# Kernel tuning notes

Measured on AMD Instinct MI355X. Metric: run time of the kernel, lower is better.

The kernel has to match this reference:

```python
import jax, jax.numpy as jnp
import numpy as np

D_MODEL = 1024
N_HEADS = 16
D_FF = 4096
N_EXPERTS = 8
B, S = 4, 1024
HEAD_DIM = D_MODEL // N_HEADS

# H4 simple roots (normalized), fixed buffer
_PHI = (1.0 + np.sqrt(5.0)) / 2.0
_R = np.array([[1, -1, 0, 0], [0, 1, -1, 0], [0, 0, 1, 0], [-0.5, 0.5, 0.5, _PHI / 2]], dtype=np.float32)
_R = _R / np.linalg.norm(_R, axis=1, keepdims=True)
ROOTS = jnp.asarray(_R)  # (4, 4)

# chamber -> (expert1, expert2) lookup, fixed buffer
_P = []
for i in range(16):
    e1 = i % N_EXPERTS
    e2 = (i // 2 + 1) % N_EXPERTS
    if e1 == e2:
        e2 = (e2 + 1) % N_EXPERTS
    _P.append([e1, e2])
CHAMBER_TO_EXPERTS = jnp.asarray(np.array(_P, dtype=np.int32))  # (16, 2)


def layer_norm(x, g, b, eps=1e-5):
    mu = jnp.mean(x, axis=-1, keepdims=True)
    var = jnp.mean(jnp.square(x - mu), axis=-1, keepdims=True)
    return (x - mu) / jnp.sqrt(var + eps) * g + b


def ternary_linear(x, w):
    # ternary quantization with STE; forward uses quantized weights
    alpha = jnp.mean(jnp.abs(w))
    w_tern = jnp.sign(w) * (jnp.abs(w) > 0.5 * alpha).astype(w.dtype)
    w_q = w + jax.lax.stop_gradient(w_tern - w)
    # per-token RMS normalization of the input
    rms = jnp.linalg.norm(x, axis=-1, keepdims=True) / np.sqrt(x.shape[-1])
    x_norm = x / (rms + 1e-8)
    return x_norm @ w_q.T


def setup_inputs() -> dict:
    key = jax.random.key(0)
    ks = jax.random.split(key, 8)
    init = lambda k, shape: jax.random.normal(k, shape, jnp.float32) * 0.02
    return {
        "x": jax.random.normal(ks[0], (B, S, D_MODEL), jnp.float32),
        "g1": jnp.ones((D_MODEL,), jnp.float32),
        "b1": jnp.zeros((D_MODEL,), jnp.float32),
        "g2": jnp.ones((D_MODEL,), jnp.float32),
        "b2": jnp.zeros((D_MODEL,), jnp.float32),
        "in_w": init(ks[1], (3 * D_MODEL, D_MODEL)),
        "in_b": jnp.zeros((3 * D_MODEL,), jnp.float32),
        "out_w": init(ks[2], (D_MODEL, D_MODEL)),
        "out_b": jnp.zeros((D_MODEL,), jnp.float32),
        "router_w": init(ks[3], (4, D_MODEL)),
        "up_w": init(ks[4], (N_EXPERTS, D_FF, D_MODEL)),
        "down_w": init(ks[5], (N_EXPERTS, D_MODEL, D_FF)),
    }


def reference(x, g1, b1, g2, b2, in_w, in_b, out_w, out_b, router_w, up_w, down_w):
    batch, seq, d = x.shape

    # ---- attention sublayer ----
    residual = x
    h = layer_norm(x, g1, b1)
    qkv = h @ in_w.T + in_b  # (B,S,3D)
    q, k, v = jnp.split(qkv, 3, axis=-1)
    def heads(t):
        return t.reshape(batch, seq, N_HEADS, HEAD_DIM).transpose(0, 2, 1, 3)
    q, k, v = heads(q), heads(k), heads(v)
    scores = jnp.einsum("bhqd,bhkd->bhqk", q, k) / np.sqrt(HEAD_DIM)
    attn = jax.nn.softmax(scores, axis=-1)
    o = jnp.einsum("bhqk,bhkd->bhqd", attn, v)
    o = o.transpose(0, 2, 1, 3).reshape(batch, seq, d)
    x = o @ out_w.T + out_b + residual

    # ---- MoE sublayer ----
    residual = x
    x_norm = layer_norm(x, g2, b2)

    # geometric router
    h4 = x_norm @ router_w.T  # (B,S,4)
    h4 = h4 / jnp.maximum(jnp.linalg.norm(h4, axis=-1, keepdims=True), 1e-12)
    dots = h4 @ ROOTS.T  # (B,S,4)
    bits = (dots >= 0).astype(jnp.int32)
    chamber = bits[..., 0] + 2 * bits[..., 1] + 4 * bits[..., 2] + 8 * bits[..., 3]
    expert_idx = CHAMBER_TO_EXPERTS[chamber]  # (B,S,2)
    confidence = jnp.min(jnp.abs(dots), axis=-1)
    w1 = 0.5 + 0.3 * jax.nn.sigmoid(confidence)
    w2 = 1.0 - w1

    # dense masked combine: per-token weight is 0 for non-routed experts,
    # so this computes the same math as the masked gather/scatter loop
    out = jnp.zeros_like(x_norm)
    for e in range(N_EXPERTS):
        w_e = w1 * (expert_idx[..., 0] == e) + w2 * (expert_idx[..., 1] == e)  # (B,S)
        h_e = ternary_linear(x_norm, up_w[e])
        h_e = jax.nn.gelu(h_e, approximate=False)
        y_e = ternary_linear(h_e, down_w[e])
        out = out + y_e * w_e[..., None]

    return out + residual
```

## Files before the change

### kernel.cpp

```cpp
#include <hip/hip_runtime.h>
#include <math.h>

#define TOK 4096
#define DM 1024
#define DFF 4096
#define MATSZ 4194304
#define PADROWS 9216
#define PADTILES 72

typedef unsigned short u16;
typedef unsigned int   u32;
typedef __attribute__((ext_vector_type(8))) __bf16 bf16x8;
typedef __attribute__((ext_vector_type(4))) float  f32x4;
typedef __attribute__((ext_vector_type(4))) int    i32x4;
typedef __attribute__((ext_vector_type(4))) float  f4v;

#define GLD16(gp, lp) __builtin_amdgcn_global_load_lds( \
    (const __attribute__((address_space(1))) void*)(gp), \
    (__attribute__((address_space(3))) void*)(lp), 16, 0, 0)

__device__ __forceinline__ float b2f(u16 u){ return __uint_as_float(((u32)u)<<16); }
__device__ __forceinline__ u16 f2b(float f){
  u32 i = __float_as_uint(f);
  u32 r = i + 0x7fffu + ((i>>16)&1u);
  return (u16)(r>>16);
}
__device__ __forceinline__ void unpack8(uint4 rw, float* dst){
  u32 u0=rw.x,u1=rw.y,u2=rw.z,u3=rw.w;
  dst[0]=__uint_as_float(u0<<16); dst[1]=__uint_as_float(u0&0xffff0000u);
  dst[2]=__uint_as_float(u1<<16); dst[3]=__uint_as_float(u1&0xffff0000u);
  dst[4]=__uint_as_float(u2<<16); dst[5]=__uint_as_float(u2&0xffff0000u);
  dst[6]=__uint_as_float(u3<<16); dst[7]=__uint_as_float(u3&0xffff0000u);
}
__device__ __forceinline__ float block_reduce_sum256(float v, float* red){
  #pragma unroll
  for (int off=32; off>0; off>>=1) v += __shfl_down(v, off);
  __syncthreads();
  if ((threadIdx.x & 63)==0) red[threadIdx.x>>6] = v;
  __syncthreads();
  return red[0]+red[1]+red[2]+red[3];
}
__device__ __forceinline__ float block_reduce_max256(float v, float* red){
  #pragma unroll
  for (int off=32; off>0; off>>=1) v = fmaxf(v, __shfl_down(v, off));
  __syncthreads();
  if ((threadIdx.x & 63)==0) red[threadIdx.x>>6] = v;
  __syncthreads();
  return fmaxf(fmaxf(red[0],red[1]), fmaxf(red[2],red[3]));
}

__global__ __launch_bounds__(256) void k_absum1(const float* __restrict__ up, const float* __restrict__ dn,
                                                float* __restrict__ partials){
  const int b = blockIdx.x;
  const size_t f4i = (size_t)b*2048;
  const f4v* s4 = (b < 4096) ? ((const f4v*)up + f4i) : ((const f4v*)dn + (f4i - 8388608));
  const int tid = threadIdx.x;
  float a0=0.f,a1=0.f,a2=0.f,a3=0.f;
  #pragma unroll
  for (int i=0;i<2;i++){
    f4v v0 = __builtin_nontemporal_load(s4 + i*1024 + tid);
    f4v v1 = __builtin_nontemporal_load(s4 + i*1024 + tid + 256);
    f4v v2 = __builtin_nontemporal_load(s4 + i*1024 + tid + 512);
    f4v v3 = __builtin_nontemporal_load(s4 + i*1024 + tid + 768);
    a0 += fabsf(v0[0])+fabsf(v0[1])+fabsf(v0[2])+fabsf(v0[3]);
    a1 += fabsf(v1[0])+fabsf(v1[1])+fabsf(v1[2])+fabsf(v1[3]);
    a2 += fabsf(v2[0])+fabsf(v2[1])+fabsf(v2[2])+fabsf(v2[3]);
    a3 += fabsf(v3[0])+fabsf(v3[1])+fabsf(v3[2])+fabsf(v3[3]);
  }
  __shared__ float red[4];
  float tot = block_reduce_sum256((a0+a1)+(a2+a3), red);
  if (tid==0) partials[b]=tot;
}
__global__ void k_absum2(const float* __restrict__ partials, float* __restrict__ thr,
                         int* __restrict__ counts, int* __restrict__ counts2){
  const int t=threadIdx.x;
  const int m=t>>4, k=t&15;
  float s=0.f;
  for (int i=0;i<32;i++) s += partials[m*512 + k + i*16];
  s += __shfl_xor(s,1); s += __shfl_xor(s,2); s += __shfl_xor(s,4); s += __shfl_xor(s,8);
  if (k==0) thr[m]=0.5f*s/4194304.0f;
  if (t>=224 && t<232) counts[t-224]=0;
  if (t>=232 && t<240) counts2[t-232]=0;
}
__global__ __launch_bounds__(256) void k_ternarize(const float* __restrict__ up, const float* __restrict__ dn,
                                                   const float* __restrict__ thr, signed char* __restrict__ tern){
  const int nvec = 16777216;
  for (int i0 = blockIdx.x*1024 + threadIdx.x; i0 < nvec; i0 += gridDim.x*1024){
    const int i1 = i0 + 256, i2 = i0 + 512, i3 = i0 + 768;
    f4v w0 = (i0 < 8388608) ? __builtin_nontemporal_load((const f4v*)up + i0) : __builtin_nontemporal_load((const f4v*)dn + (i0-8388608));
    f4v w1 = (i1 < 8388608) ? __builtin_nontemporal_load((const f4v*)up + i1) : __builtin_nontemporal_load((const f4v*)dn + (i1-8388608));
    f4v w2 = (i2 < 8388608) ? __builtin_nontemporal_load((const f4v*)up + i2) : __builtin_nontemporal_load((const f4v*)dn + (i2-8388608));
    f4v w3 = (i3 < 8388608) ? __builtin_nontemporal_load((const f4v*)up + i3) : __builtin_nontemporal_load((const f4v*)dn + (i3-8388608));
    float t0 = thr[(int)(((size_t)i0*4)>>22)];
    float t1 = thr[(int)(((size_t)i1*4)>>22)];
    float t2 = thr[(int)(((size_t)i2*4)>>22)];
    float t3 = thr[(int)(((size_t)i3*4)>>22)];
    char4 c0, c1, c2, c3;
    c0.x=(fabsf(w0[0])>t0)?(w0[0]>0.f?1:-1):0; c0.y=(fabsf(w0[1])>t0)?(w0[1]>0.f?1:-1):0;
    c0.z=(fabsf(w0[2])>t0)?(w0[2]>0.f?1:-1):0; c0.w=(fabsf(w0[3])>t0)?(w0[3]>0.f?1:-1):0;
    c1.x=(fabsf(w1[0])>t1)?(w1[0]>0.f?1:-1):0; c1.y=(fabsf(w1[1])>t1)?(w1[1]>0.f?1:-1):0;
    c1.z=(fabsf(w1[2])>t1)?(w1[2]>0.f?1:-1):0; c1.w=(fabsf(w1[3])>t1)?(w1[3]>0.f?1:-1):0;
    c2.x=(fabsf(w2[0])>t2)?(w2[0]>0.f?1:-1):0; c2.y=(fabsf(w2[1])>t2)?(w2[1]>0.f?1:-1):0;
    c2.z=(fabsf(w2[2])>t2)?(w2[2]>0.f?1:-1):0; c2.w=(fabsf(w2[3])>t2)?(w2[3]>0.f?1:-1):0;
    c3.x=(fabsf(w3[0])>t3)?(w3[0]>0.f?1:-1):0; c3.y=(fabsf(w3[1])>t3)?(w3[1]>0.f?1:-1):0;
    c3.z=(fabsf(w3[2])>t3)?(w3[2]>0.f?1:-1):0; c3.w=(fabsf(w3[3])>t3)?(w3[3]>0.f?1:-1):0;
    *(char4*)(tern+(size_t)i0*4) = c0;
    *(char4*)(tern+(size_t)i1*4) = c1;
    *(char4*)(tern+(size_t)i2*4) = c2;
    *(char4*)(tern+(size_t)i3*4) = c3;
  }
}
__global__ __launch_bounds__(256) void k_f2b(const float* __restrict__ s, u16* __restrict__ d, int n4){
  int i = blockIdx.x*256+threadIdx.x;
  if (i<n4){
    float4 v=((const float4*)s)[i];
    ushort4 o; o.x=f2b(v.x); o.y=f2b(v.y); o.z=f2b(v.z); o.w=f2b(v.w);
    ((ushort4*)d)[i]=o;
  }
}

__global__ __launch_bounds__(256) void k_ln1(const float* __restrict__ x, const float* __restrict__ g,
                                             const float* __restrict__ b, u16* __restrict__ h){
  __shared__ float red[4];
  const int t=blockIdx.x, tid=threadIdx.x;
  float4 xv = ((const float4*)(x + (size_t)t*DM))[tid];
  float s  = xv.x+xv.y+xv.z+xv.w;
  float sq = xv.x*xv.x+xv.y*xv.y+xv.z*xv.z+xv.w*xv.w;
  float sum  = block_reduce_sum256(s, red);
  float sums = block_reduce_sum256(sq, red);
  float mu = sum*(1.0f/DM);
  float var = sums*(1.0f/DM) - mu*mu;
  float rstd = rsqrtf(var+1e-5f);
  float4 gv = ((const float4*)g)[tid];
  float4 bv = ((const float4*)b)[tid];
  ushort4 pk;
  pk.x = f2b((xv.x-mu)*rstd*gv.x+bv.x);
  pk.y = f2b((xv.y-mu)*rstd*gv.y+bv.y);
  pk.z = f2b((xv.z-mu)*rstd*gv.z+bv.z);
  pk.w = f2b((xv.w-mu)*rstd*gv.w+bv.w);
  ((ushort4*)(h + (size_t)t*DM))[tid] = pk;
}

template<int MODE>
__global__ __launch_bounds__(256) void k_gemm(const u16* __restrict__ A, const u16* __restrict__ B,
                                              int K, int ldc, const float* __restrict__ bias,
                                              const float* __restrict__ resid, void* __restrict__ Cout,
                                              u16* __restrict__ vT){
  __shared__ u16 As[2][128*32];
  __shared__ u16 Bs[2][128*32];
  const int tid = threadIdx.x;
  const int w = tid>>6, lane = tid&63;
  const int m0 = blockIdx.y*128, n0 = blockIdx.x*128;

  const int sr = lane>>2, ss = lane&3;
  const int ra0 = w*32 + sr, ra1 = ra0 + 16;
  const int kb0 = (ss ^ ((ra0>>1)&3))<<3;
  const int kb1 = (ss ^ ((ra1>>1)&3))<<3;
  const u16* pa0 = A + (size_t)(m0+ra0)*K + kb0;
  const u16* pa1 = A + (size_t)(m0+ra1)*K + kb1;
  const u16* pb0 = B + (size_t)(n0+ra0)*K + kb0;
  const u16* pb1 = B + (size_t)(n0+ra1)*K + kb1;
  const int lo0 = (w*32)*32, lo1 = lo0 + 16*32;

  const int wm = w>>1, wn = w&1;
  const int lr = lane&15, sl = lane>>4;
  int offA[4], offB[4];
  #pragma unroll
  for (int m=0;m<4;m++){ int r = wm*64 + m*16 + lr; offA[m] = r*64 + ((sl ^ ((r>>1)&3))<<4); }
  #pragma unroll
  for (int n=0;n<4;n++){ int r = wn*64 + n*16 + lr; offB[n] = r*64 + ((sl ^ ((r>>1)&3))<<4); }

  f32x4 acc[4][4] = {};
  const int NT = K>>5;
  GLD16(pa0, &As[0][lo0]); GLD16(pa1, &As[0][lo1]);
  GLD16(pb0, &Bs[0][lo0]); GLD16(pb1, &Bs[0][lo1]);
  pa0+=32; pa1+=32; pb0+=32; pb1+=32;
  __syncthreads();

  for (int t=0;t<NT;t++){
    if (t+1<NT){
      const int nb=(t+1)&1;
      GLD16(pa0, &As[nb][lo0]); GLD16(pa1, &As[nb][lo1]);
      GLD16(pb0, &Bs[nb][lo0]); GLD16(pb1, &Bs[nb][lo1]);
      pa0+=32; pa1+=32; pb0+=32; pb1+=32;
    }
    const char* Ab = (const char*)As[t&1];
    const char* Bb = (const char*)Bs[t&1];
    bf16x8 af[4], bfv[4];
    #pragma unroll
    for (int m=0;m<4;m++) af[m] = *(const bf16x8*)(Ab + offA[m]);
    #pragma unroll
    for (int n=0;n<4;n++) bfv[n] = *(const bf16x8*)(Bb + offB[n]);
    #pragma unroll
    for (int m=0;m<4;m++)
      #pragma unroll
      for (int n=0;n<4;n++)
        acc[m][n] = __builtin_amdgcn_mfma_f32_16x16x32_bf16(af[m], bfv[n], acc[m][n], 0, 0, 0);
    __syncthreads();
  }

  const int rowg = lane>>4;
  #pragma unroll
  for (int m=0;m<4;m++){
    const int rbase = m0 + wm*64 + m*16 + rowg*4;
    #pragma unroll
    for (int n=0;n<4;n++){
      const int col = n0 + wn*64 + n*16 + lr;
      if (MODE==2){
        u16 pk4[4];
        #pragma unroll
        for (int j=0;j<4;j++){
          float v = acc[m][n][j] + bias[col];
          pk4[j] = f2b(v);
          ((u16*)Cout)[(size_t)(rbase+j)*ldc + col] = pk4[j];
        }
        if (col >= 2048){
          const int d = col-2048, hd = d>>6, dd = d&63;
          const int bb = rbase>>10, s = rbase&1023;
          uint2 pk; pk.x = (u32)pk4[0] | ((u32)pk4[1]<<16); pk.y = (u32)pk4[2] | ((u32)pk4[3]<<16);
          *(uint2*)(vT + (((size_t)((bb*16+hd)*64+dd))<<10) + s) = pk;
        }
      } else {
        #pragma unroll
        for (int j=0;j<4;j++){
          const size_t ci = (size_t)(rbase+j)*ldc + col;
          ((float*)Cout)[ci] = acc[m][n][j] + bias[col] + resid[ci];
        }
      }
    }
  }
}

template<bool GATHER>
__global__ __launch_bounds__(256) void k_gemm8(const signed char* __restrict__ A, const signed char* __restrict__ Ball,
                                               int K, int ldc,
                                               const int* __restrict__ tile2e, const int* __restrict__ rowmap,
                                               const float* __restrict__ rscale, u16* __restrict__ Cout){
  int e = tile2e[blockIdx.y];
  if (e < 0) return;
  const signed char* Bp = Ball + (size_t)e * MATSZ;
  __shared__ signed char As[2][128*64];
  __shared__ signed char Bs[2][128*64];
  const int tid = threadIdx.x;
  const int w = tid>>6, lane = tid&63;
  const int m0 = blockIdx.y*128, n0 = blockIdx.x*128;

  const int sr = lane>>2, ss = lane&3;
  const int ra0 = w*32 + sr, ra1 = ra0 + 16;
  const int kb0 = (ss ^ ((ra0>>1)&3))<<4;
  const int kb1 = (ss ^ ((ra1>>1)&3))<<4;
  const signed char *pa0, *pa1;
  if (GATHER){
    int t0 = rowmap[m0+ra0]; if (t0<0) t0 = 0;
    int t1 = rowmap[m0+ra1]; if (t1<0) t1 = 0;
    pa0 = A + (size_t)t0*K + kb0;
    pa1 = A + (size_t)t1*K + kb1;
  } else {
    pa0 = A + (size_t)(m0+ra0)*K + kb0;
    pa1 = A + (size_t)(m0+ra1)*K + kb1;
  }
  const signed char* pb0 = Bp + (size_t)(n0+ra0)*K + kb0;
  const signed char* pb1 = Bp + (size_t)(n0+ra1)*K + kb1;
  const int lo0 = (w*32)*64, lo1 = lo0 + 16*64;

  const int wm = w>>1, wn = w&1;
  const int lr = lane&15, sl = lane>>4;
  int offA[4], offB[4];
  #pragma unroll
  for (int m=0;m<4;m++){ int r = wm*64 + m*16 + lr; offA[m] = r*64 + ((sl ^ ((r>>1)&3))<<4); }
  #pragma unroll
  for (int n=0;n<4;n++){ int r = wn*64 + n*16 + lr; offB[n] = r*64 + ((sl ^ ((r>>1)&3))<<4); }

  i32x4 acc[4][4] = {};
  const int NT = K>>6;
  GLD16(pa0, &As[0][lo0]); GLD16(pa1, &As[0][lo1]);
  GLD16(pb0, &Bs[0][lo0]); GLD16(pb1, &Bs[0][lo1]);
  pa0+=64; pa1+=64; pb0+=64; pb1+=64;
  __syncthreads();

  for (int t=0;t<NT;t++){
    if (t+1<NT){
      const int nb=(t+1)&1;
      GLD16(pa0, &As[nb][lo0]); GLD16(pa1, &As[nb][lo1]);
      GLD16(pb0, &Bs[nb][lo0]); GLD16(pb1, &Bs[nb][lo1]);
      pa0+=64; pa1+=64; pb0+=64; pb1+=64;
    }
    const char* Ab = (const char*)As[t&1];
    const char* Bb = (const char*)Bs[t&1];
    i32x4 af[4], bfv[4];
    #pragma unroll
    for (int m=0;m<4;m++) af[m] = *(const i32x4*)(Ab + offA[m]);
    #pragma unroll
    for (int n=0;n<4;n++) bfv[n] = *(const i32x4*)(Bb + offB[n]);
    #pragma unroll
    for (int m=0;m<4;m++)
      #pragma unroll
      for (int n=0;n<4;n++)
        acc[m][n] = __builtin_amdgcn_mfma_i32_16x16x64_i8(af[m], bfv[n], acc[m][n], 0, 0, 0);
    __syncthreads();
  }

  const int rowg = lane>>4;
  #pragma unroll
  for (int m=0;m<4;m++){
    const int rbase = m0 + wm*64 + m*16 + rowg*4;
    #pragma unroll
    for (int n=0;n<4;n++){
      const int col = n0 + wn*64 + n*16 + lr;
      #pragma unroll
      for (int j=0;j<4;j++){
        float v = (float)acc[m][n][j] * rscale[rbase+j];
        Cout[(size_t)(rbase+j)*ldc + col] = f2b(v);
      }
    }
  }
}

__global__ __launch_bounds__(256) void k_attn_mfma(const u16* __restrict__ qkv, const u16* __restrict__ vT,
                                                   u16* __restrict__ ob){
  __shared__ u16 Ks[2][64*64];
  __shared__ u16 Vs[2][64*64];
  __shared__ u16 Pa[4*16*64];
  const int qt=blockIdx.x, hh=blockIdx.y, bb=blockIdx.z;
  const int tid=threadIdx.x, w=tid>>6, lane=tid&63;
  const int g=lane>>4, lr=lane&15;
  const int srow8=lane>>3, sslot=lane&7;
  const float RTHR = 11.5f;

  bf16x8 qa[2];
  {
    const u16* qp = qkv + ((size_t)(bb*1024 + qt*64 + w*16 + lr))*3072 + hh*64 + g*8;
    #pragma unroll
    for (int c=0;c<2;c++){
      uint4 raw = *(const uint4*)(qp + c*32);
      float tv[8]; unpack8(raw,tv);
      union { u16 s[8]; bf16x8 v; } qq;
      #pragma unroll
      for (int i=0;i<8;i++) qq.s[i] = f2b(tv[i]*0.18033688f);
      qa[c] = qq.v;
    }
  }

  float mrow[4], lrow[4];
  #pragma unroll
  for (int j=0;j<4;j++){ mrow[j]=-1e30f; lrow[j]=0.f; }
  f32x4 acc_o[4] = {};

  char* pbuf = (char*)Pa + (w<<11);

  const int row0 = w*16 + srow8, row1 = row0 + 8;
  const int fs0 = (sslot ^ (row0&7))<<3;
  const int fs1 = (sslot ^ (row1&7))<<3;
  const int ldso0 = (w*16)*64, ldso1 = (w*16+8)*64;

  {
    const u16* gk0 = qkv + ((size_t)(bb*1024 + row0))*3072 + 1024 + hh*64 + fs0;
    const u16* gk1 = qkv + ((size_t)(bb*1024 + row1))*3072 + 1024 + hh*64 + fs1;
    GLD16(gk0, &Ks[0][ldso0]); GLD16(gk1, &Ks[0][ldso1]);
    const u16* gv0 = vT + ((size_t)((bb*16+hh)*64 + row0))*1024 + fs0;
    const u16* gv1 = vT + ((size_t)((bb*16+hh)*64 + row1))*1024 + fs1;
    GLD16(gv0, &Vs[0][ldso0]); GLD16(gv1, &Vs[0][ldso1]);
  }
  __syncthreads();

  for (int kt=0; kt<16; ++kt){
    if (kt+1<16){
      const int nb=(kt+1)&1;
      const u16* gk0 = qkv + ((size_t)(bb*1024 + (kt+1)*64 + row0))*3072 + 1024 + hh*64 + fs0;
      const u16* gk1 = qkv + ((size_t)(bb*1024 + (kt+1)*64 + row1))*3072 + 1024 + hh*64 + fs1;
      GLD16(gk0, &Ks[nb][ldso0]); GLD16(gk1, &Ks[nb][ldso1]);
      const u16* gv0 = vT + ((size_t)((bb*16+hh)*64 + row0))*1024 + (kt+1)*64 + fs0;
      const u16* gv1 = vT + ((size_t)((bb*16+hh)*64 + row1))*1024 + (kt+1)*64 + fs1;
      GLD16(gv0, &Vs[nb][ldso0]); GLD16(gv1, &Vs[nb][ldso1]);
    }
    const char* Kb = (const char*)Ks[kt&1];
    const char* Vb = (const char*)Vs[kt&1];

    f32x4 sacc[4] = {};
    #pragma unroll
    for (int ct=0; ct<4; ct++){
      const int kv = ct*16 + lr;
      const char* krow = Kb + kv*128;
      bf16x8 kb0 = *(const bf16x8*)(krow + (((g  ) ^ (kv&7))<<4));
      bf16x8 kb1 = *(const bf16x8*)(krow + (((4+g) ^ (kv&7))<<4));
      sacc[ct] = __builtin_amdgcn_mfma_f32_16x16x32_bf16(qa[0], kb0, sacc[ct], 0,0,0);
      sacc[ct] = __builtin_amdgcn_mfma_f32_16x16x32_bf16(qa[1], kb1, sacc[ct], 0,0,0);
    }

    float vmx[4]; bool okl = true;
    #pragma unroll
    for (int j=0;j<4;j++){
      vmx[j] = fmaxf(fmaxf(sacc[0][j],sacc[1][j]), fmaxf(sacc[2][j],sacc[3][j]));
      okl = okl && (vmx[j]-mrow[j] <= RTHR);
    }
    float psum[4] = {0.f,0.f,0.f,0.f};
    if (__all((int)okl)){
      #pragma unroll
      for (int ct=0; ct<4; ct++){
        #pragma unroll
        for (int j=0;j<4;j++){
          float p = exp2f(sacc[ct][j]-mrow[j]);
          psum[j] += p;
          const int q = g*4+j, k = ct*16+lr;
          *(u16*)(pbuf + q*128 + (((k>>3) ^ (q&7))<<4) + ((k&7)<<1)) = f2b(p);
        }
      }
      #pragma unroll
      for (int j=0;j<4;j++){
        float s = psum[j];
        s += __shfl_xor(s,1); s += __shfl_xor(s,2); s += __shfl_xor(s,4); s += __shfl_xor(s,8);
        lrow[j] += s;
      }
    } else {
      float mnew[4], corr[4];
      #pragma unroll
      for (int j=0;j<4;j++){
        float v = vmx[j];
        v = fmaxf(v, __shfl_xor(v,1));
        v = fmaxf(v, __shfl_xor(v,2));
        v = fmaxf(v, __shfl_xor(v,4));
        v = fmaxf(v, __shfl_xor(v,8));
        mnew[j] = fmaxf(mrow[j], v);
        corr[j] = exp2f(mrow[j]-mnew[j]);
        mrow[j] = mnew[j];
      }
      #pragma unroll
      for (int ct=0; ct<4; ct++){
        #pragma unroll
        for (int j=0;j<4;j++){
          float p = exp2f(sacc[ct][j]-mrow[j]);
          psum[j] += p;
          const int q = g*4+j, k = ct*16+lr;
          *(u16*)(pbuf + q*128 + (((k>>3) ^ (q&7))<<4) + ((k&7)<<1)) = f2b(p);
        }
      }
      #pragma unroll
      for (int j=0;j<4;j++){
        float s = psum[j];
        s += __shfl_xor(s,1); s += __shfl_xor(s,2); s += __shfl_xor(s,4); s += __shfl_xor(s,8);
        lrow[j] = lrow[j]*corr[j] + s;
      }
      #pragma unroll
      for (int ctd=0; ctd<4; ctd++)
        #pragma unroll
        for (int j=0;j<4;j++) acc_o[ctd][j] *= corr[j];
    }

    #pragma unroll
    for (int c=0;c<2;c++){
      bf16x8 pa = *(const bf16x8*)(pbuf + lr*128 + (((c*4+g) ^ (lr&7))<<4));
      #pragma unroll
      for (int ctd=0; ctd<4; ctd++){
        const int d = ctd*16 + lr;
        bf16x8 vb = *(const bf16x8*)(Vb + d*128 + (((c*4+g) ^ (d&7))<<4));
        acc_o[ctd] = __builtin_amdgcn_mfma_f32_16x16x32_bf16(pa, vb, acc_o[ctd], 0,0,0);
      }
    }
    __syncthreads();
  }

  #pragma unroll
  for (int j=0;j<4;j++){
    const float inv = 1.0f/lrow[j];
    const int row = bb*1024 + qt*64 + w*16 + g*4 + j;
    u16* op = ob + (size_t)row*DM + hh*64 + lr;
    #pragma unroll
    for (int ctd=0; ctd<4; ctd++) op[ctd*16] = f2b(acc_o[ctd][j]*inv);
  }
}

__global__ __launch_bounds__(256) void k_ln2_router(const float* __restrict__ xa, const float* __restrict__ g,
                                                    const float* __restrict__ b, const float* __restrict__ rw,
                                                    signed char* __restrict__ xn8, int* __restrict__ eidx,
                                                    float* __restrict__ w1o, float* __restrict__ sbc){
  __shared__ float red[4];
  const int t=blockIdx.x, tid=threadIdx.x;
  float4 xv = ((const float4*)(xa + (size_t)t*DM))[tid];
  float s  = xv.x+xv.y+xv.z+xv.w;
  float sq = xv.x*xv.x+xv.y*xv.y+xv.z*xv.z+xv.w*xv.w;
  float sum  = block_reduce_sum256(s, red);
  float sums = block_reduce_sum256(sq, red);
  float mu = sum*(1.0f/DM);
  float var = sums*(1.0f/DM) - mu*mu;
  float rstd = rsqrtf(var+1e-5f);
  float4 gv = ((const float4*)g)[tid];
  float4 bv = ((const float4*)b)[tid];
  float y0=(xv.x-mu)*rstd*gv.x+bv.x;
  float y1=(xv.y-mu)*rstd*gv.y+bv.y;
  float y2=(xv.z-mu)*rstd*gv.z+bv.z;
  float y3=(xv.w-mu)*rstd*gv.w+bv.w;
  float4 r0=((const float4*)(rw+0*DM))[tid];
  float4 r1=((const float4*)(rw+1*DM))[tid];
  float4 r2=((const float4*)(rw+2*DM))[tid];
  float4 r3=((const float4*)(rw+3*DM))[tid];
  float nsq = y0*y0+y1*y1+y2*y2+y3*y3;
  float d0 = y0*r0.x+y1*r0.y+y2*r0.z+y3*r0.w;
  float d1 = y0*r1.x+y1*r1.y+y2*r1.z+y3*r1.w;
  float d2 = y0*r2.x+y1*r2.y+y2*r2.z+y3*r2.w;
  float d3 = y0*r3.x+y1*r3.y+y2*r3.z+y3*r3.w;
  float am = fmaxf(fmaxf(fabsf(y0),fabsf(y1)), fmaxf(fabsf(y2),fabsf(y3)));
  float AM = block_reduce_max256(am, red);
  float SQ = block_reduce_sum256(nsq, red);
  float D0 = block_reduce_sum256(d0, red);
  float D1 = block_reduce_sum256(d1, red);
  float D2 = block_reduce_sum256(d2, red);
  float D3 = block_reduce_sum256(d3, red);
  float qs = fmaxf(AM, 1e-12f) * (1.0f/127.0f);
  float inv = 1.0f/qs;
  char4 c;
  c.x = (signed char)__float2int_rn(y0*inv);
  c.y = (signed char)__float2int_rn(y1*inv);
  c.z = (signed char)__float2int_rn(y2*inv);
  c.w = (signed char)__float2int_rn(y3*inv);
  ((char4*)(xn8 + (size_t)t*DM))[tid] = c;
  if (tid==0){
    float n = fmaxf(sqrtf(D0*D0+D1*D1+D2*D2+D3*D3), 1e-12f);
    float h0=D0/n, h1=D1/n, h2=D2/n, h3=D3/n;
    float dot0 = 0.70710678f*(h0-h1);
    float dot1 = 0.70710678f*(h1-h2);
    float dot2 = h2;
    float dot3 = (-0.5f*h0+0.5f*h1+0.5f*h2+0.80901699f*h3)*0.8437966f;
    int ch = (int)(dot0>=0.f) + 2*(int)(dot1>=0.f) + 4*(int)(dot2>=0.f) + 8*(int)(dot3>=0.f);
    int e1 = ch & 7;
    int e2 = ((ch>>1)+1) & 7;
    if (e1==e2) e2=(e2+1)&7;
    float conf = fminf(fminf(fabsf(dot0),fabsf(dot1)), fminf(fabsf(dot2),fabsf(dot3)));
    eidx[2*t]=e1; eidx[2*t+1]=e2;
    w1o[t]=0.5f + 0.3f/(1.0f+__expf(-conf));
    sbc[t]= qs / (sqrtf(SQ*(1.0f/DM))+1e-8f);
  }
}

__global__ void k_count(const int* __restrict__ eidx, int* __restrict__ counts){
  int t = blockIdx.x*256+threadIdx.x;
  if (t<TOK){ atomicAdd(&counts[eidx[2*t]],1); atomicAdd(&counts[eidx[2*t+1]],1); }
}
__global__ void k_offsets(const int* __restrict__ counts, int* __restrict__ offs, int* __restrict__ tile2e,
                          int* __restrict__ rowmap, float* __restrict__ srow, int* __restrict__ ptot){
  const int tid=threadIdx.x;
  if (tid==0){
    int off=0;
    for (int e=0;e<8;e++){
      offs[e]=off;
      int pad = ((counts[e]+127)>>7)<<7;
      int t0=off>>7, t1=(off+pad)>>7;
      for (int tt=t0;tt<t1;tt++) tile2e[tt]=e;
      off+=pad;
    }
    offs[8]=off; *ptot=off;
    for (int tt=off>>7; tt<PADTILES; tt++) tile2e[tt]=-1;
  }
  for (int i=tid;i<PADROWS;i+=blockDim.x){ rowmap[i]=-1; srow[i]=0.f; }
}
__global__ void k_scatter(const int* __restrict__ eidx, const int* __restrict__ offs, int* __restrict__ counts2,
                          int* __restrict__ rowmap, int* __restrict__ tokrow,
                          const float* __restrict__ sbc, float* __restrict__ srow){
  int t = blockIdx.x*256+threadIdx.x;
  if (t<TOK){
    int e1=eidx[2*t], e2=eidx[2*t+1];
    float s = sbc[t];
    int p1 = atomicAdd(&counts2[e1],1);
    int r1 = offs[e1]+p1; rowmap[r1]=t; srow[r1]=s; tokrow[2*t]=r1;
    int p2 = atomicAdd(&counts2[e2],1);
    int r2 = offs[e2]+p2; rowmap[r2]=t; srow[r2]=s; tokrow[2*t+1]=r2;
  }
}

__global__ __launch_bounds__(256) void k_gelu_rms(const u16* __restrict__ he, signed char* __restrict__ he8,
                                                  float* __restrict__ qd, const int* __restrict__ ptot){
  const int row = blockIdx.x;
  if (row >= *ptot) return;
  const u16* p = he + (size_t)row*DFF;
  const int tid=threadIdx.x;
  uint4 rw0 = ((const uint4*)p)[2*tid];
  uint4 rw1 = ((const uint4*)p)[2*tid+1];
  float v[16];
  unpack8(rw0, v); unpack8(rw1, v+8);
  float sq=0.f;
  #pragma unroll
  for (int q=0;q<16;q++){
    float xg = v[q];
    float ge = 0.5f*xg*(1.0f+erff(xg*0.70710678f));
    v[q]=ge; sq += ge*ge;
  }
  __shared__ float red[4];
  float SQ = block_reduce_sum256(sq, red);
  float s = 1.0f/(sqrtf(SQ*(1.0f/DFF))+1e-8f);
  float am = 0.f;
  #pragma unroll
  for (int q=0;q<16;q++){ v[q]*=s; am = fmaxf(am, fabsf(v[q])); }
  float AM = block_reduce_max256(am, red);
  float q8 = fmaxf(AM, 1e-12f) * (1.0f/127.0f);
  float inv = 1.0f/q8;
  union { signed char c[16]; uint4 u; } pk;
  #pragma unroll
  for (int q=0;q<16;q++) pk.c[q] = (signed char)__float2int_rn(v[q]*inv);
  ((uint4*)(he8 + (size_t)row*DFF))[tid] = pk.u;
  if (tid==0) qd[row] = q8;
}

__global__ __launch_bounds__(256) void k_combine(const float* __restrict__ xa, const u16* __restrict__ y,
                                                 const int* __restrict__ tokrow, const float* __restrict__ w1,
                                                 float* __restrict__ out){
  const int t=blockIdx.x, tid=threadIdx.x;
  const int r1=tokrow[2*t], r2=tokrow[2*t+1];
  const float a = w1[t], bw = 1.0f-a;
  float4 xv = ((const float4*)(xa + (size_t)t*DM))[tid];
  ushort4 y1 = ((const ushort4*)(y + (size_t)r1*DM))[tid];
  ushort4 y2 = ((const ushort4*)(y + (size_t)r2*DM))[tid];
  float4 o;
  o.x = xv.x + a*b2f(y1.x) + bw*b2f(y2.x);
  o.y = xv.y + a*b2f(y1.y) + bw*b2f(y2.y);
  o.z = xv.z + a*b2f(y1.z) + bw*b2f(y2.z);
  o.w = xv.w + a*b2f(y1.w) + bw*b2f(y2.w);
  ((float4*)(out + (size_t)t*DM))[tid] = o;
}

extern "C" void kernel_launch(void* const* d_in, const int* in_sizes, int n_in,
                              void* d_out, int out_size, void* d_ws, size_t ws_size,
                              hipStream_t stream){
  (void)in_sizes; (void)n_in; (void)out_size; (void)ws_size;
  const float* x    = (const float*)d_in[0];
  const float* g1   = (const float*)d_in[1];
  const float* b1   = (const float*)d_in[2];
  const float* g2   = (const float*)d_in[3];
  const float* b2   = (const float*)d_in[4];
  const float* in_w = (const float*)d_in[5];
  const float* in_b = (const float*)d_in[6];
  const float* out_w= (const float*)d_in[7];
  const float* out_b= (const float*)d_in[8];
  const float* rw   = (const float*)d_in[9];
  const float* up_w = (const float*)d_in[10];
  const float* dn_w = (const float*)d_in[11];
  float* out = (float*)d_out;

  char* base = (char*)d_ws; size_t off=0;
  auto alloc = [&](size_t bytes)->char*{ char* p = base+off; off=(off+bytes+255)&~(size_t)255; return p; };
  u16* h      = (u16*)alloc((size_t)TOK*DM*2);
  u16* qkv    = (u16*)alloc((size_t)TOK*3072*2);
  u16* ob     = (u16*)alloc((size_t)TOK*DM*2);
  float* xattn= (float*)alloc((size_t)TOK*DM*4);
  signed char* xn8 = (signed char*)alloc((size_t)TOK*DM);
  signed char* tern8 = (signed char*)alloc((size_t)16*MATSZ);
  u16* wbf_in = (u16*)alloc((size_t)3145728*2);
  u16* wbf_out= (u16*)alloc((size_t)1048576*2);
  u16* vT     = (u16*)alloc((size_t)4*16*64*1024*2);
  u16* he     = (u16*)alloc((size_t)PADROWS*DFF*2);
  signed char* he8 = (signed char*)alloc((size_t)PADROWS*DFF);
  u16* y      = (u16*)alloc((size_t)PADROWS*DM*2);
  float* partials = (float*)alloc(8192*4);
  float* thr  = (float*)alloc(64);
  int* counts = (int*)alloc(32);
  int* counts2= (int*)alloc(32);
  int* offs   = (int*)alloc(64);
  int* ptot   = (int*)alloc(64);
  int* eidx   = (int*)alloc((size_t)TOK*2*4);
  float* w1b  = (float*)alloc((size_t)TOK*4);
  float* sbc  = (float*)alloc((size_t)TOK*4);
  float* srow = (float*)alloc((size_t)PADROWS*4);
  float* qd   = (float*)alloc((size_t)PADROWS*4);
  int* tokrow = (int*)alloc((size_t)TOK*2*4);
  int* rowmap = (int*)alloc((size_t)PADROWS*4);
  int* tile2e = (int*)alloc(PADTILES*4);

  k_absum1<<<8192,256,0,stream>>>(up_w, dn_w, partials);
  k_absum2<<<1,256,0,stream>>>(partials, thr, counts, counts2);
  k_ternarize<<<8192,256,0,stream>>>(up_w, dn_w, thr, tern8);
  k_f2b<<<3072,256,0,stream>>>(in_w, wbf_in, 786432);
  k_f2b<<<1024,256,0,stream>>>(out_w, wbf_out, 262144);
  k_ln1<<<TOK,256,0,stream>>>(x, g1, b1, h);
  k_gemm<2><<<dim3(24,32),256,0,stream>>>(h, wbf_in, 1024, 3072, in_b, nullptr, qkv, vT);
  k_attn_mfma<<<dim3(16,16,4),256,0,stream>>>(qkv, vT, ob);
  k_gemm<3><<<dim3(8,32),256,0,stream>>>(ob, wbf_out, 1024, 1024, out_b, x, xattn, nullptr);
  k_ln2_router<<<TOK,256,0,stream>>>(xattn, g2, b2, rw, xn8, eidx, w1b, sbc);
  k_count<<<16,256,0,stream>>>(eidx, counts);
  k_offsets<<<1,256,0,stream>>>(counts, offs, tile2e, rowmap, srow, ptot);
  k_scatter<<<16,256,0,stream>>>(eidx, offs, counts2, rowmap, tokrow, sbc, srow);
  k_gemm8<true><<<dim3(32,PADTILES),256,0,stream>>>(xn8, tern8, 1024, 4096,
      tile2e, rowmap, srow, he);
  k_gelu_rms<<<PADROWS,256,0,stream>>>(he, he8, qd, ptot);
  k_gemm8<false><<<dim3(8,PADTILES),256,0,stream>>>(he8, tern8 + (size_t)8*MATSZ, 4096, 1024,
      tile2e, nullptr, qd, y);
  k_combine<<<TOK,256,0,stream>>>(xattn, y, tokrow, w1b, out);
}
```

Baseline: 497.8 us.

## Triple-buffer GEMM LDS pipelines, raise attention MFMA priority, fuse expert counting

Both the bf16 and int8 GEMM kernels move from double to triple LDS buffering. They issue two tiles ahead and replace the two barriers per iteration with one explicit vmcnt wait plus an s_barrier, aiming to hide more global-load latency. The attention kernel wraps its MFMA sections in s_setprio to favour matrix issue. The separate expert-count kernel is removed and its atomics move into the router kernel, saving one launch. The extra LDS raises per-block shared memory use and may lower occupancy, and the hand-written waitcnt adds correctness risk.

```diff
diff --git a/kernel.cpp b/kernel.cpp
--- a/kernel.cpp
+++ b/kernel.cpp
@@ -146,8 +146,8 @@
                                               int K, int ldc, const float* __restrict__ bias,
                                               const float* __restrict__ resid, void* __restrict__ Cout,
                                               u16* __restrict__ vT){
-  __shared__ u16 As[2][128*32];
-  __shared__ u16 Bs[2][128*32];
+  __shared__ u16 As[3][128*32];
+  __shared__ u16 Bs[3][128*32];
   const int tid = threadIdx.x;
   const int w = tid>>6, lane = tid&63;
   const int m0 = blockIdx.y*128, n0 = blockIdx.x*128;
@@ -175,17 +175,22 @@
   GLD16(pa0, &As[0][lo0]); GLD16(pa1, &As[0][lo1]);
   GLD16(pb0, &Bs[0][lo0]); GLD16(pb1, &Bs[0][lo1]);
   pa0+=32; pa1+=32; pb0+=32; pb1+=32;
-  __syncthreads();
-
+  GLD16(pa0, &As[1][lo0]); GLD16(pa1, &As[1][lo1]);
+  GLD16(pb0, &Bs[1][lo0]); GLD16(pb1, &Bs[1][lo1]);
+  pa0+=32; pa1+=32; pb0+=32; pb1+=32;
+
+  int cur=0, nx2=2;
   for (int t=0;t<NT;t++){
-    if (t+1<NT){
-      const int nb=(t+1)&1;
-      GLD16(pa0, &As[nb][lo0]); GLD16(pa1, &As[nb][lo1]);
-      GLD16(pb0, &Bs[nb][lo0]); GLD16(pb1, &Bs[nb][lo1]);
+    if (t+1<NT) asm volatile("s_waitcnt vmcnt(4) lgkmcnt(0)" ::: "memory");
+    else        asm volatile("s_waitcnt vmcnt(0) lgkmcnt(0)" ::: "memory");
+    __builtin_amdgcn_s_barrier();
+    if (t+2<NT){
+      GLD16(pa0, &As[nx2][lo0]); GLD16(pa1, &As[nx2][lo1]);
+      GLD16(pb0, &Bs[nx2][lo0]); GLD16(pb1, &Bs[nx2][lo1]);
       pa0+=32; pa1+=32; pb0+=32; pb1+=32;
     }
-    const char* Ab = (const char*)As[t&1];
-    const char* Bb = (const char*)Bs[t&1];
+    const char* Ab = (const char*)As[cur];
+    const char* Bb = (const char*)Bs[cur];
     bf16x8 af[4], bfv[4];
     #pragma unroll
     for (int m=0;m<4;m++) af[m] = *(const bf16x8*)(Ab + offA[m]);
@@ -196,7 +201,8 @@
       #pragma unroll
       for (int n=0;n<4;n++)
         acc[m][n] = __builtin_amdgcn_mfma_f32_16x16x32_bf16(af[m], bfv[n], acc[m][n], 0, 0, 0);
-    __syncthreads();
+    cur = (cur==2)?0:cur+1;
+    nx2 = (nx2==2)?0:nx2+1;
   }
 
   const int rowg = lane>>4;
@@ -239,8 +245,8 @@
   int e = tile2e[blockIdx.y];
   if (e < 0) return;
   const signed char* Bp = Ball + (size_t)e * MATSZ;
-  __shared__ signed char As[2][128*64];
-  __shared__ signed char Bs[2][128*64];
+  __shared__ signed char As[3][128*64];
+  __shared__ signed char Bs[3][128*64];
   const int tid = threadIdx.x;
   const int w = tid>>6, lane = tid&63;
   const int m0 = blockIdx.y*128, n0 = blockIdx.x*128;
@@ -276,17 +282,22 @@
   GLD16(pa0, &As[0][lo0]); GLD16(pa1, &As[0][lo1]);
   GLD16(pb0, &Bs[0][lo0]); GLD16(pb1, &Bs[0][lo1]);
   pa0+=64; pa1+=64; pb0+=64; pb1+=64;
-  __syncthreads();
-
+  GLD16(pa0, &As[1][lo0]); GLD16(pa1, &As[1][lo1]);
+  GLD16(pb0, &Bs[1][lo0]); GLD16(pb1, &Bs[1][lo1]);
+  pa0+=64; pa1+=64; pb0+=64; pb1+=64;
+
+  int cur=0, nx2=2;
   for (int t=0;t<NT;t++){
-    if (t+1<NT){
-      const int nb=(t+1)&1;
-      GLD16(pa0, &As[nb][lo0]); GLD16(pa1, &As[nb][lo1]);
-      GLD16(pb0, &Bs[nb][lo0]); GLD16(pb1, &Bs[nb][lo1]);
+    if (t+1<NT) asm volatile("s_waitcnt vmcnt(4) lgkmcnt(0)" ::: "memory");
+    else        asm volatile("s_waitcnt vmcnt(0) lgkmcnt(0)" ::: "memory");
+    __builtin_amdgcn_s_barrier();
+    if (t+2<NT){
+      GLD16(pa0, &As[nx2][lo0]); GLD16(pa1, &As[nx2][lo1]);
+      GLD16(pb0, &Bs[nx2][lo0]); GLD16(pb1, &Bs[nx2][lo1]);
       pa0+=64; pa1+=64; pb0+=64; pb1+=64;
     }
-    const char* Ab = (const char*)As[t&1];
-    const char* Bb = (const char*)Bs[t&1];
+    const char* Ab = (const char*)As[cur];
+    const char* Bb = (const char*)Bs[cur];
     i32x4 af[4], bfv[4];
     #pragma unroll
     for (int m=0;m<4;m++) af[m] = *(const i32x4*)(Ab + offA[m]);
@@ -297,7 +308,8 @@
       #pragma unroll
       for (int n=0;n<4;n++)
         acc[m][n] = __builtin_amdgcn_mfma_i32_16x16x64_i8(af[m], bfv[n], acc[m][n], 0, 0, 0);
-    __syncthreads();
+    cur = (cur==2)?0:cur+1;
+    nx2 = (nx2==2)?0:nx2+1;
   }
 
   const int rowg = lane>>4;
@@ -377,6 +389,7 @@
     const char* Vb = (const char*)Vs[kt&1];
 
     f32x4 sacc[4] = {};
+    __builtin_amdgcn_s_setprio(1);
     #pragma unroll
     for (int ct=0; ct<4; ct++){
       const int kv = ct*16 + lr;
@@ -386,6 +399,7 @@
       sacc[ct] = __builtin_amdgcn_mfma_f32_16x16x32_bf16(qa[0], kb0, sacc[ct], 0,0,0);
       sacc[ct] = __builtin_amdgcn_mfma_f32_16x16x32_bf16(qa[1], kb1, sacc[ct], 0,0,0);
     }
+    __builtin_amdgcn_s_setprio(0);
 
     float vmx[4]; bool okl = true;
     #pragma unroll
@@ -446,6 +460,7 @@
         for (int j=0;j<4;j++) acc_o[ctd][j] *= corr[j];
     }
 
+    __builtin_amdgcn_s_setprio(1);
     #pragma unroll
     for (int c=0;c<2;c++){
       bf16x8 pa = *(const bf16x8*)(pbuf + lr*128 + (((c*4+g) ^ (lr&7))<<4));
@@ -456,6 +471,7 @@
         acc_o[ctd] = __builtin_amdgcn_mfma_f32_16x16x32_bf16(pa, vb, acc_o[ctd], 0,0,0);
       }
     }
+    __builtin_amdgcn_s_setprio(0);
     __syncthreads();
   }
 
@@ -472,7 +488,8 @@
 __global__ __launch_bounds__(256) void k_ln2_router(const float* __restrict__ xa, const float* __restrict__ g,
                                                     const float* __restrict__ b, const float* __restrict__ rw,
                                                     signed char* __restrict__ xn8, int* __restrict__ eidx,
-                                                    float* __restrict__ w1o, float* __restrict__ sbc){
+                                                    float* __restrict__ w1o, float* __restrict__ sbc,
+                                                    int* __restrict__ counts){
   __shared__ float red[4];
   const int t=blockIdx.x, tid=threadIdx.x;
   float4 xv = ((const float4*)(xa + (size_t)t*DM))[tid];
@@ -526,15 +543,12 @@
     if (e1==e2) e2=(e2+1)&7;
     float conf = fminf(fminf(fabsf(dot0),fabsf(dot1)), fminf(fabsf(dot2),fabsf(dot3)));
     eidx[2*t]=e1; eidx[2*t+1]=e2;
+    atomicAdd(&counts[e1],1); atomicAdd(&counts[e2],1);
     w1o[t]=0.5f + 0.3f/(1.0f+__expf(-conf));
     sbc[t]= qs / (sqrtf(SQ*(1.0f/DM))+1e-8f);
   }
 }
 
-__global__ void k_count(const int* __restrict__ eidx, int* __restrict__ counts){
-  int t = blockIdx.x*256+threadIdx.x;
-  if (t<TOK){ atomicAdd(&counts[eidx[2*t]],1); atomicAdd(&counts[eidx[2*t+1]],1); }
-}
 __global__ void k_offsets(const int* __restrict__ counts, int* __restrict__ offs, int* __restrict__ tile2e,
                           int* __restrict__ rowmap, float* __restrict__ srow, int* __restrict__ ptot){
   const int tid=threadIdx.x;
@@ -672,8 +686,7 @@
   k_gemm<2><<<dim3(24,32),256,0,stream>>>(h, wbf_in, 1024, 3072, in_b, nullptr, qkv, vT);
   k_attn_mfma<<<dim3(16,16,4),256,0,stream>>>(qkv, vT, ob);
   k_gemm<3><<<dim3(8,32),256,0,stream>>>(ob, wbf_out, 1024, 1024, out_b, x, xattn, nullptr);
-  k_ln2_router<<<TOK,256,0,stream>>>(xattn, g2, b2, rw, xn8, eidx, w1b, sbc);
-  k_count<<<16,256,0,stream>>>(eidx, counts);
+  k_ln2_router<<<TOK,256,0,stream>>>(xattn, g2, b2, rw, xn8, eidx, w1b, sbc, counts);
   k_offsets<<<1,256,0,stream>>>(counts, offs, tile2e, rowmap, srow, ptot);
   k_scatter<<<16,256,0,stream>>>(eidx, offs, counts2, rowmap, tokrow, sbc, srow);
   k_gemm8<true><<<dim3(32,PADTILES),256,0,stream>>>(xn8, tern8, 1024, 4096,
```

New measurement: 546.7 us. 9.8% more time.
